# Kernel optimization log

Hardware: AMD Instinct MI355X
Metric: run time of the kernel (lower is better)

Reference implementation:

```python
import jax, jax.numpy as jnp
import numpy as np

N, D_IN, D_BLOCK, D_OUT, E, K = 65536, 128, 256, 128, 8, 2


def setup_inputs() -> dict:
    key = jax.random.key(0)
    ks = jax.random.split(key, 8)
    s_in = 1.0 / np.sqrt(D_IN)
    s_h = 1.0 / np.sqrt(D_BLOCK)
    return {
        "x": jax.random.normal(ks[0], (N, D_IN), jnp.float32),
        "Wg": jax.random.normal(ks[1], (D_IN, E), jnp.float32) * s_in,
        "W1": jax.random.normal(ks[2], (E, D_IN, D_BLOCK), jnp.float32) * s_in,
        "b1": jax.random.normal(ks[3], (E, D_BLOCK), jnp.float32) * 0.01,
        "W2": jax.random.normal(ks[4], (E, D_BLOCK, D_BLOCK), jnp.float32) * s_h,
        "b2": jax.random.normal(ks[5], (E, D_BLOCK), jnp.float32) * 0.01,
        "Wo": jax.random.normal(ks[6], (D_BLOCK, D_OUT), jnp.float32) * s_h,
        "bo": jax.random.normal(ks[7], (D_OUT,), jnp.float32) * 0.01,
    }


def reference(x, Wg, W1, b1, W2, b2, Wo, bo):
    # Router: linear gate -> top-k -> softmax over the k selected logits,
    # scattered back to a dense [N, E] combine-weight matrix (zeros elsewhere).
    logits = x @ Wg                                   # [N, E]
    topv, topi = jax.lax.top_k(logits, K)             # [N, K]
    w_topk = jax.nn.softmax(topv, axis=-1)            # [N, K]
    onehot = jax.nn.one_hot(topi, E, dtype=x.dtype)   # [N, K, E]
    weights = jnp.einsum("nk,nke->ne", w_topk, onehot)  # [N, E]

    # Expert MLPs (n_blocks=2, ReLU, dropout=0 at eval), computed for all
    # experts over all tokens; unselected experts have weight 0, so the
    # weighted combine reproduces the original masked gather/scatter math.
    h = jax.nn.relu(jnp.einsum("nd,edh->enh", x, W1) + b1[:, None, :])   # [E,N,H]
    h = jax.nn.relu(jnp.einsum("enh,ehg->eng", h, W2) + b2[:, None, :])  # [E,N,H]
    y = jnp.einsum("enh,ho->eno", h, Wo) + bo                             # [E,N,O]

    # Weighted scatter-add combine: outs[n] = sum_e weights[n,e] * y[e,n]
    return jnp.einsum("ne,eno->no", weights, y)
```

## Files before the change

### kernel.cpp

```cpp
#include <hip/hip_runtime.h>
#include <math.h>

typedef unsigned short ushort_t;
typedef __attribute__((ext_vector_type(8))) short bf16x8;
typedef __attribute__((ext_vector_type(4))) float f32x4;
typedef __attribute__((ext_vector_type(8))) unsigned short u16x8;

#define N_TOK 65536
#define DIN 128
#define HD 256
#define DOUT 128
#define NEXP 8
#define MT 64
#define MAX_TILES (N_TOK / MT)

__device__ __forceinline__ unsigned short f2bf(float f) {
    union { float f; unsigned int i; } v; v.f = f;
    unsigned int i = v.i;
    return (unsigned short)((i + 0x7FFFu + ((i >> 16) & 1u)) >> 16);
}

__global__ void pack_weights(const float* __restrict__ W1,
                             const float* __restrict__ W2,
                             const float* __restrict__ Wo,
                             ushort_t* __restrict__ wt1f,
                             ushort_t* __restrict__ wt2f,
                             ushort_t* __restrict__ wotf) {
    int id = blockIdx.x * 256 + threadIdx.x;
    const float* src; ushort_t* dst; int Nn, ksteps, c;
    if (id < 32768) {
        int e = id >> 12; c = id & 4095;
        Nn = HD; ksteps = 4; src = W1 + (size_t)e * DIN * HD; dst = wt1f + (size_t)id * 8;
    } else if (id < 98304) {
        int t = id - 32768; int e = t >> 13; c = t & 8191;
        Nn = HD; ksteps = 8; src = W2 + (size_t)e * HD * HD; dst = wt2f + (size_t)t * 8;
    } else {
        int t = id - 98304; c = t;
        Nn = DOUT; ksteps = 8; src = Wo; dst = wotf + (size_t)t * 8;
    }
    int L = c & 63; int kc = c >> 6;
    int kstep = kc % ksteps; int ntile = kc / ksteps;
    int q = L >> 4, m = L & 15;
    int n = ntile * 16 + m; int k0 = kstep * 32 + q * 8;
    u16x8 v;
#pragma unroll
    for (int j = 0; j < 8; j++) v[j] = f2bf(src[(size_t)(k0 + j) * Nn + n]);
    *(u16x8*)dst = v;
}

#define RT_BLOCK 512
#define RT_TPB 64
__global__ __launch_bounds__(RT_BLOCK)
void router_kernel(const float* __restrict__ x,
                   const float* __restrict__ Wg,
                   int* __restrict__ counts,
                   int* __restrict__ list_tok,
                   float* __restrict__ list_w) {
    __shared__ float wgsT[NEXP * 132];
    __shared__ int lcnt[NEXP];
    __shared__ int lbase[NEXP];
    int tid = threadIdx.x;
    if (tid < NEXP) lcnt[tid] = 0;
    for (int i = tid; i < DIN * NEXP; i += RT_BLOCK) {
        int e = i & 7, k = i >> 3;
        wgsT[e * 132 + k] = Wg[i];
    }
    __syncthreads();

    int e = tid & 7;
    int tl = tid >> 3;
    int n = blockIdx.x * RT_TPB + tl;
    const float4* xr = (const float4*)(x + (size_t)n * DIN);
    const float4* wv4 = (const float4*)(wgsT + e * 132);
    float lg = 0.f;
#pragma unroll
    for (int kk = 0; kk < 32; kk++) {
        float4 xv = xr[kk];
        float4 wv = wv4[kk];
        lg += xv.x * wv.x;
        lg += xv.y * wv.y;
        lg += xv.z * wv.z;
        lg += xv.w * wv.w;
    }
    float v0 = lg; int e0 = e;
#pragma unroll
    for (int d = 1; d < 8; d <<= 1) {
        float ov = __shfl_xor(v0, d, 64);
        int oe = __shfl_xor(e0, d, 64);
        if (ov > v0 || (ov == v0 && oe < e0)) { v0 = ov; e0 = oe; }
    }
    float mv = (e == e0) ? -3.0e38f : lg;
    float v1 = mv; int e1 = e;
#pragma unroll
    for (int d = 1; d < 8; d <<= 1) {
        float ov = __shfl_xor(v1, d, 64);
        int oe = __shfl_xor(e1, d, 64);
        if (ov > v1 || (ov == v1 && oe < e1)) { v1 = ov; e1 = oe; }
    }
    float t = expf(v1 - v0);
    float inv = 1.0f / (1.0f + t);
    float w0 = inv, w1 = t * inv;

    bool writer = (e == 0);
    int p0 = 0, p1 = 0;
    if (writer) {
        p0 = atomicAdd(&lcnt[e0], 1);
        p1 = atomicAdd(&lcnt[e1], 1);
    }
    __syncthreads();
    if (tid < NEXP) lbase[tid] = atomicAdd(&counts[tid], lcnt[tid]);
    __syncthreads();
    if (writer) {
        int q0 = lbase[e0] + p0;
        list_tok[e0 * N_TOK + q0] = n;
        list_w[e0 * N_TOK + q0] = w0;
        int q1 = lbase[e1] + p1;
        list_tok[e1 * N_TOK + q1] = n;
        list_w[e1 * N_TOK + q1] = w1;
    }
}

__global__ void init_out(const float* __restrict__ bo, float* __restrict__ out) {
    int gid = blockIdx.x * 256 + threadIdx.x;
    float4 b = ((const float4*)bo)[gid & 31];
    ((float4*)out)[gid] = b;
}

__global__ __launch_bounds__(256, 3)
void expert_kernel(const float* __restrict__ x,
                   const int* __restrict__ counts,
                   const int* __restrict__ list_tok,
                   const float* __restrict__ list_w,
                   const ushort_t* __restrict__ wt1f,
                   const ushort_t* __restrict__ wt2f,
                   const ushort_t* __restrict__ wotf,
                   const float* __restrict__ b1,
                   const float* __restrict__ b2,
                   float* __restrict__ out) {
    int e = blockIdx.x & 7;
    int tile = blockIdx.x >> 3;
    int cnt = counts[e];
    int base = tile * MT;
    if (base >= cnt) return;
    int rows = cnt - base; if (rows > MT) rows = MT;

    __shared__ __align__(16) ushort_t bufA[8192];
    __shared__ __align__(16) ushort_t bufH[16384];
    __shared__ int toks_s[MT];
    __shared__ float wts_s[MT];

    int tid = threadIdx.x;
    int lane = tid & 63;
    int w = tid >> 6;
    int q = lane >> 4;
    int mcol = lane & 15;

    if (tid < MT) {
        int rr = tid < rows ? tid : rows - 1;
        toks_s[tid] = list_tok[(size_t)e * N_TOK + base + rr];
        wts_s[tid] = list_w[(size_t)e * N_TOK + base + rr];
    }
    for (int c = tid; c < 1024; c += 256) {
        int row = c >> 4;
        int kchunk = c & 15;
        int rr = row < rows ? row : rows - 1;
        int tok = list_tok[(size_t)e * N_TOK + base + rr];
        const float4* src = (const float4*)(x + (size_t)tok * DIN + kchunk * 8);
        float4 lo = src[0], hi = src[1];
        u16x8 v;
        v[0] = f2bf(lo.x); v[1] = f2bf(lo.y); v[2] = f2bf(lo.z); v[3] = f2bf(lo.w);
        v[4] = f2bf(hi.x); v[5] = f2bf(hi.y); v[6] = f2bf(hi.z); v[7] = f2bf(hi.w);
        int kstep = kchunk >> 2, qq = kchunk & 3;
        int dchunk = (kstep * 4 + (row >> 4)) * 64 + qq * 16 + (row & 15);
        ((u16x8*)bufA)[dchunk] = v;
    }
    __syncthreads();

    const bf16x8* Albs = (const bf16x8*)bufA;
    const bf16x8* Hlbs = (const bf16x8*)bufH;

    f32x4 acc[4][4];
#pragma unroll
    for (int mt = 0; mt < 4; mt++)
#pragma unroll
        for (int nt = 0; nt < 4; nt++) acc[mt][nt] = (f32x4){0.f, 0.f, 0.f, 0.f};
    const bf16x8* B1 = (const bf16x8*)(wt1f + (size_t)e * 4096 * 8);
#pragma unroll
    for (int kstep = 0; kstep < 4; kstep++) {
        bf16x8 a[4];
#pragma unroll
        for (int mt = 0; mt < 4; mt++) a[mt] = Albs[(kstep * 4 + mt) * 64 + lane];
#pragma unroll
        for (int nt = 0; nt < 4; nt++) {
            bf16x8 b = B1[((w * 4 + nt) * 4 + kstep) * 64 + lane];
#pragma unroll
            for (int mt = 0; mt < 4; mt++)
                acc[mt][nt] = __builtin_amdgcn_mfma_f32_16x16x32_bf16(a[mt], b, acc[mt][nt], 0, 0, 0);
        }
    }
#pragma unroll
    for (int nt = 0; nt < 4; nt++) {
        int nn = (w * 4 + nt) * 16 + mcol;
        float bias = b1[e * HD + nn];
        int kstep = nn >> 5, qq = (nn >> 3) & 3, jj = nn & 7;
#pragma unroll
        for (int mt = 0; mt < 4; mt++) {
#pragma unroll
            for (int r = 0; r < 4; r++) {
                float v = acc[mt][nt][r] + bias;
                v = v > 0.f ? v : 0.f;
                int chunk = (kstep * 4 + mt) * 64 + qq * 16 + q * 4 + r;
                bufH[chunk * 8 + jj] = f2bf(v);
            }
        }
    }
    __syncthreads();

    f32x4 acc2[4][4];
#pragma unroll
    for (int mt = 0; mt < 4; mt++)
#pragma unroll
        for (int nt = 0; nt < 4; nt++) acc2[mt][nt] = (f32x4){0.f, 0.f, 0.f, 0.f};
    const bf16x8* B2 = (const bf16x8*)(wt2f + (size_t)e * 8192 * 8);
#pragma unroll
    for (int kstep = 0; kstep < 8; kstep++) {
        bf16x8 a[4];
#pragma unroll
        for (int mt = 0; mt < 4; mt++) a[mt] = Hlbs[(kstep * 4 + mt) * 64 + lane];
#pragma unroll
        for (int nt = 0; nt < 4; nt++) {
            bf16x8 b = B2[((w * 4 + nt) * 8 + kstep) * 64 + lane];
#pragma unroll
            for (int mt = 0; mt < 4; mt++)
                acc2[mt][nt] = __builtin_amdgcn_mfma_f32_16x16x32_bf16(a[mt], b, acc2[mt][nt], 0, 0, 0);
        }
    }
    __syncthreads();
#pragma unroll
    for (int nt = 0; nt < 4; nt++) {
        int nn = (w * 4 + nt) * 16 + mcol;
        float bias = b2[e * HD + nn];
        int kstep = nn >> 5, qq = (nn >> 3) & 3, jj = nn & 7;
#pragma unroll
        for (int mt = 0; mt < 4; mt++) {
#pragma unroll
            for (int r = 0; r < 4; r++) {
                float v = acc2[mt][nt][r] + bias;
                v = v > 0.f ? v : 0.f;
                int chunk = (kstep * 4 + mt) * 64 + qq * 16 + q * 4 + r;
                bufH[chunk * 8 + jj] = f2bf(v);
            }
        }
    }
    __syncthreads();

    f32x4 acc3[4][2];
#pragma unroll
    for (int mt = 0; mt < 4; mt++)
#pragma unroll
        for (int nt = 0; nt < 2; nt++) acc3[mt][nt] = (f32x4){0.f, 0.f, 0.f, 0.f};
    const bf16x8* B3 = (const bf16x8*)wotf;
#pragma unroll
    for (int kstep = 0; kstep < 8; kstep++) {
        bf16x8 a[4];
#pragma unroll
        for (int mt = 0; mt < 4; mt++) a[mt] = Hlbs[(kstep * 4 + mt) * 64 + lane];
#pragma unroll
        for (int nt = 0; nt < 2; nt++) {
            bf16x8 b = B3[((w * 2 + nt) * 8 + kstep) * 64 + lane];
#pragma unroll
            for (int mt = 0; mt < 4; mt++)
                acc3[mt][nt] = __builtin_amdgcn_mfma_f32_16x16x32_bf16(a[mt], b, acc3[mt][nt], 0, 0, 0);
        }
    }
#pragma unroll
    for (int mt = 0; mt < 4; mt++) {
#pragma unroll
        for (int r = 0; r < 4; r++) {
            int row = mt * 16 + q * 4 + r;
            if (row < rows) {
                int tok = toks_s[row];
                float wgt = wts_s[row];
                float* dst = out + (size_t)tok * DOUT;
#pragma unroll
                for (int nt = 0; nt < 2; nt++) {
                    int col = (w * 2 + nt) * 16 + mcol;
                    atomicAdd(&dst[col], wgt * acc3[mt][nt][r]);
                }
            }
        }
    }
}

extern "C" void kernel_launch(void* const* d_in, const int* in_sizes, int n_in,
                              void* d_out, int out_size, void* d_ws, size_t ws_size,
                              hipStream_t stream) {
    const float* x  = (const float*)d_in[0];
    const float* Wg = (const float*)d_in[1];
    const float* W1 = (const float*)d_in[2];
    const float* b1 = (const float*)d_in[3];
    const float* W2 = (const float*)d_in[4];
    const float* b2 = (const float*)d_in[5];
    const float* Wo = (const float*)d_in[6];
    const float* bo = (const float*)d_in[7];
    float* out = (float*)d_out;

    char* ws = (char*)d_ws;
    size_t off = 0;
    int* counts    = (int*)(ws + off);    off += 256;
    int* list_tok  = (int*)(ws + off);    off += (size_t)NEXP * N_TOK * 4;
    float* list_w  = (float*)(ws + off);  off += (size_t)NEXP * N_TOK * 4;
    ushort_t* wt1f = (ushort_t*)(ws + off); off += (size_t)NEXP * DIN * HD * 2;
    ushort_t* wt2f = (ushort_t*)(ws + off); off += (size_t)NEXP * HD * HD * 2;
    ushort_t* wotf = (ushort_t*)(ws + off); off += (size_t)HD * DOUT * 2;

    hipMemsetAsync(counts, 0, 256, stream);
    pack_weights<<<400, 256, 0, stream>>>(W1, W2, Wo, wt1f, wt2f, wotf);
    router_kernel<<<N_TOK / RT_TPB, RT_BLOCK, 0, stream>>>(x, Wg, counts, list_tok, list_w);
    init_out<<<(N_TOK * DOUT / 4) / 256, 256, 0, stream>>>(bo, out);
    expert_kernel<<<NEXP * MAX_TILES, 256, 0, stream>>>(x, counts, list_tok, list_w,
                                                        wt1f, wt2f, wotf, b1, b2, out);
}
```

Before: 199.6 us.

## Split K across router lanes and use 2x2 warp tiling in expert GEMMs

The router now has each of 8 lanes per token read a distinct 16-float slice of x and compute partial dot products for all 8 experts, then reduce with xor shuffles. Before, all 8 lanes read the full token row. This cuts redundant global reads of x, and the block shrinks to 256 threads with 32 tokens each. The expert kernel switches from warps owning N-slices across all four M-tiles to a 2x2 warp grid: each warp now loads 2 A fragments and 8 B fragments per k-step instead of 4 A and 4 B. That moves per-warp traffic from shared memory to global/L2 weight loads and changes the output atomic pattern.

Measured after the change: 254.5 us. +27.5%, slower.

```diff
diff --git a/kernel.cpp b/kernel.cpp
--- a/kernel.cpp
+++ b/kernel.cpp
@@ -48,9 +48,8 @@
     *(u16x8*)dst = v;
 }
 
-#define RT_BLOCK 512
-#define RT_TPB 64
-__global__ __launch_bounds__(RT_BLOCK)
+#define RT_TPB 32
+__global__ __launch_bounds__(256)
 void router_kernel(const float* __restrict__ x,
                    const float* __restrict__ Wg,
                    int* __restrict__ counts,
@@ -61,47 +60,49 @@
     __shared__ int lbase[NEXP];
     int tid = threadIdx.x;
     if (tid < NEXP) lcnt[tid] = 0;
-    for (int i = tid; i < DIN * NEXP; i += RT_BLOCK) {
+    for (int i = tid; i < DIN * NEXP; i += 256) {
         int e = i & 7, k = i >> 3;
         wgsT[e * 132 + k] = Wg[i];
     }
     __syncthreads();
 
-    int e = tid & 7;
+    int s = tid & 7;
     int tl = tid >> 3;
     int n = blockIdx.x * RT_TPB + tl;
-    const float4* xr = (const float4*)(x + (size_t)n * DIN);
-    const float4* wv4 = (const float4*)(wgsT + e * 132);
-    float lg = 0.f;
-#pragma unroll
-    for (int kk = 0; kk < 32; kk++) {
-        float4 xv = xr[kk];
-        float4 wv = wv4[kk];
-        lg += xv.x * wv.x;
-        lg += xv.y * wv.y;
-        lg += xv.z * wv.z;
-        lg += xv.w * wv.w;
-    }
-    float v0 = lg; int e0 = e;
+
+    const float4* xr = (const float4*)(x + (size_t)n * DIN + s * 16);
+    float4 xv[4];
+#pragma unroll
+    for (int j = 0; j < 4; j++) xv[j] = xr[j];
+
+    float lg[NEXP];
+#pragma unroll
+    for (int e = 0; e < NEXP; e++) {
+        const float4* wp = (const float4*)(wgsT + e * 132 + s * 16);
+        float a = 0.f;
+#pragma unroll
+        for (int j = 0; j < 4; j++) {
+            float4 wv = wp[j];
+            a += xv[j].x * wv.x + xv[j].y * wv.y + xv[j].z * wv.z + xv[j].w * wv.w;
+        }
+        lg[e] = a;
+    }
 #pragma unroll
     for (int d = 1; d < 8; d <<= 1) {
-        float ov = __shfl_xor(v0, d, 64);
-        int oe = __shfl_xor(e0, d, 64);
-        if (ov > v0 || (ov == v0 && oe < e0)) { v0 = ov; e0 = oe; }
-    }
-    float mv = (e == e0) ? -3.0e38f : lg;
-    float v1 = mv; int e1 = e;
-#pragma unroll
-    for (int d = 1; d < 8; d <<= 1) {
-        float ov = __shfl_xor(v1, d, 64);
-        int oe = __shfl_xor(e1, d, 64);
-        if (ov > v1 || (ov == v1 && oe < e1)) { v1 = ov; e1 = oe; }
-    }
+#pragma unroll
+        for (int e = 0; e < NEXP; e++) lg[e] += __shfl_xor(lg[e], d, 64);
+    }
+    int e0 = 0; float v0 = lg[0];
+#pragma unroll
+    for (int e = 1; e < NEXP; e++) if (lg[e] > v0) { v0 = lg[e]; e0 = e; }
+    int e1 = -1; float v1 = -3.0e38f;
+#pragma unroll
+    for (int e = 0; e < NEXP; e++) if (e != e0 && lg[e] > v1) { v1 = lg[e]; e1 = e; }
     float t = expf(v1 - v0);
     float inv = 1.0f / (1.0f + t);
     float w0 = inv, w1 = t * inv;
 
-    bool writer = (e == 0);
+    bool writer = (s == 0);
     int p0 = 0, p1 = 0;
     if (writer) {
         p0 = atomicAdd(&lcnt[e0], 1);
@@ -152,6 +153,8 @@
     int tid = threadIdx.x;
     int lane = tid & 63;
     int w = tid >> 6;
+    int mw = w >> 1;
+    int nw = w & 1;
     int q = lane >> 4;
     int mcol = lane & 15;
 
@@ -179,35 +182,37 @@
     const bf16x8* Albs = (const bf16x8*)bufA;
     const bf16x8* Hlbs = (const bf16x8*)bufH;
 
-    f32x4 acc[4][4];
-#pragma unroll
-    for (int mt = 0; mt < 4; mt++)
-#pragma unroll
-        for (int nt = 0; nt < 4; nt++) acc[mt][nt] = (f32x4){0.f, 0.f, 0.f, 0.f};
+    f32x4 acc[2][8];
+#pragma unroll
+    for (int mtl = 0; mtl < 2; mtl++)
+#pragma unroll
+        for (int nt = 0; nt < 8; nt++) acc[mtl][nt] = (f32x4){0.f, 0.f, 0.f, 0.f};
     const bf16x8* B1 = (const bf16x8*)(wt1f + (size_t)e * 4096 * 8);
 #pragma unroll
     for (int kstep = 0; kstep < 4; kstep++) {
-        bf16x8 a[4];
-#pragma unroll
-        for (int mt = 0; mt < 4; mt++) a[mt] = Albs[(kstep * 4 + mt) * 64 + lane];
-#pragma unroll
-        for (int nt = 0; nt < 4; nt++) {
-            bf16x8 b = B1[((w * 4 + nt) * 4 + kstep) * 64 + lane];
-#pragma unroll
-            for (int mt = 0; mt < 4; mt++)
-                acc[mt][nt] = __builtin_amdgcn_mfma_f32_16x16x32_bf16(a[mt], b, acc[mt][nt], 0, 0, 0);
-        }
-    }
-#pragma unroll
-    for (int nt = 0; nt < 4; nt++) {
-        int nn = (w * 4 + nt) * 16 + mcol;
+        bf16x8 a[2];
+#pragma unroll
+        for (int mtl = 0; mtl < 2; mtl++)
+            a[mtl] = Albs[(kstep * 4 + mw * 2 + mtl) * 64 + lane];
+#pragma unroll
+        for (int nt = 0; nt < 8; nt++) {
+            bf16x8 b = B1[((nw * 8 + nt) * 4 + kstep) * 64 + lane];
+#pragma unroll
+            for (int mtl = 0; mtl < 2; mtl++)
+                acc[mtl][nt] = __builtin_amdgcn_mfma_f32_16x16x32_bf16(a[mtl], b, acc[mtl][nt], 0, 0, 0);
+        }
+    }
+#pragma unroll
+    for (int nt = 0; nt < 8; nt++) {
+        int nn = nw * 128 + nt * 16 + mcol;
         float bias = b1[e * HD + nn];
         int kstep = nn >> 5, qq = (nn >> 3) & 3, jj = nn & 7;
 #pragma unroll
-        for (int mt = 0; mt < 4; mt++) {
+        for (int mtl = 0; mtl < 2; mtl++) {
+            int mt = mw * 2 + mtl;
 #pragma unroll
             for (int r = 0; r < 4; r++) {
-                float v = acc[mt][nt][r] + bias;
+                float v = acc[mtl][nt][r] + bias;
                 v = v > 0.f ? v : 0.f;
                 int chunk = (kstep * 4 + mt) * 64 + qq * 16 + q * 4 + r;
                 bufH[chunk * 8 + jj] = f2bf(v);
@@ -216,36 +221,38 @@
     }
     __syncthreads();
 
-    f32x4 acc2[4][4];
-#pragma unroll
-    for (int mt = 0; mt < 4; mt++)
-#pragma unroll
-        for (int nt = 0; nt < 4; nt++) acc2[mt][nt] = (f32x4){0.f, 0.f, 0.f, 0.f};
+    f32x4 acc2[2][8];
+#pragma unroll
+    for (int mtl = 0; mtl < 2; mtl++)
+#pragma unroll
+        for (int nt = 0; nt < 8; nt++) acc2[mtl][nt] = (f32x4){0.f, 0.f, 0.f, 0.f};
     const bf16x8* B2 = (const bf16x8*)(wt2f + (size_t)e * 8192 * 8);
 #pragma unroll
     for (int kstep = 0; kstep < 8; kstep++) {
-        bf16x8 a[4];
-#pragma unroll
-        for (int mt = 0; mt < 4; mt++) a[mt] = Hlbs[(kstep * 4 + mt) * 64 + lane];
-#pragma unroll
-        for (int nt = 0; nt < 4; nt++) {
-            bf16x8 b = B2[((w * 4 + nt) * 8 + kstep) * 64 + lane];
-#pragma unroll
-            for (int mt = 0; mt < 4; mt++)
-                acc2[mt][nt] = __builtin_amdgcn_mfma_f32_16x16x32_bf16(a[mt], b, acc2[mt][nt], 0, 0, 0);
-        }
-    }
-    __syncthreads();
-#pragma unroll
-    for (int nt = 0; nt < 4; nt++) {
-        int nn = (w * 4 + nt) * 16 + mcol;
+        bf16x8 a[2];
+#pragma unroll
+        for (int mtl = 0; mtl < 2; mtl++)
+            a[mtl] = Hlbs[(kstep * 4 + mw * 2 + mtl) * 64 + lane];
+#pragma unroll
+        for (int nt = 0; nt < 8; nt++) {
+            bf16x8 b = B2[((nw * 8 + nt) * 8 + kstep) * 64 + lane];
+#pragma unroll
+            for (int mtl = 0; mtl < 2; mtl++)
+                acc2[mtl][nt] = __builtin_amdgcn_mfma_f32_16x16x32_bf16(a[mtl], b, acc2[mtl][nt], 0, 0, 0);
+        }
+    }
+    __syncthreads();
+#pragma unroll
+    for (int nt = 0; nt < 8; nt++) {
+        int nn = nw * 128 + nt * 16 + mcol;
         float bias = b2[e * HD + nn];
         int kstep = nn >> 5, qq = (nn >> 3) & 3, jj = nn & 7;
 #pragma unroll
-        for (int mt = 0; mt < 4; mt++) {
+        for (int mtl = 0; mtl < 2; mtl++) {
+            int mt = mw * 2 + mtl;
 #pragma unroll
             for (int r = 0; r < 4; r++) {
-                float v = acc2[mt][nt][r] + bias;
+                float v = acc2[mtl][nt][r] + bias;
                 v = v > 0.f ? v : 0.f;
                 int chunk = (kstep * 4 + mt) * 64 + qq * 16 + q * 4 + r;
                 bufH[chunk * 8 + jj] = f2bf(v);
@@ -254,27 +261,29 @@
     }
     __syncthreads();
 
-    f32x4 acc3[4][2];
-#pragma unroll
-    for (int mt = 0; mt < 4; mt++)
-#pragma unroll
-        for (int nt = 0; nt < 2; nt++) acc3[mt][nt] = (f32x4){0.f, 0.f, 0.f, 0.f};
+    f32x4 acc3[2][4];
+#pragma unroll
+    for (int mtl = 0; mtl < 2; mtl++)
+#pragma unroll
+        for (int nt = 0; nt < 4; nt++) acc3[mtl][nt] = (f32x4){0.f, 0.f, 0.f, 0.f};
     const bf16x8* B3 = (const bf16x8*)wotf;
 #pragma unroll
     for (int kstep = 0; kstep < 8; kstep++) {
-        bf16x8 a[4];
-#pragma unroll
-        for (int mt = 0; mt < 4; mt++) a[mt] = Hlbs[(kstep * 4 + mt) * 64 + lane];
-#pragma unroll
-        for (int nt = 0; nt < 2; nt++) {
-            bf16x8 b = B3[((w * 2 + nt) * 8 + kstep) * 64 + lane];
-#pragma unroll
-            for (int mt = 0; mt < 4; mt++)
-                acc3[mt][nt] = __builtin_amdgcn_mfma_f32_16x16x32_bf16(a[mt], b, acc3[mt][nt], 0, 0, 0);
-        }
-    }
-#pragma unroll
-    for (int mt = 0; mt < 4; mt++) {
+        bf16x8 a[2];
+#pragma unroll
+        for (int mtl = 0; mtl < 2; mtl++)
+            a[mtl] = Hlbs[(kstep * 4 + mw * 2 + mtl) * 64 + lane];
+#pragma unroll
+        for (int nt = 0; nt < 4; nt++) {
+            bf16x8 b = B3[((nw * 4 + nt) * 8 + kstep) * 64 + lane];
+#pragma unroll
+            for (int mtl = 0; mtl < 2; mtl++)
+                acc3[mtl][nt] = __builtin_amdgcn_mfma_f32_16x16x32_bf16(a[mtl], b, acc3[mtl][nt], 0, 0, 0);
+        }
+    }
+#pragma unroll
+    for (int mtl = 0; mtl < 2; mtl++) {
+        int mt = mw * 2 + mtl;
 #pragma unroll
         for (int r = 0; r < 4; r++) {
             int row = mt * 16 + q * 4 + r;
@@ -283,9 +292,9 @@
                 float wgt = wts_s[row];
                 float* dst = out + (size_t)tok * DOUT;
 #pragma unroll
-                for (int nt = 0; nt < 2; nt++) {
-                    int col = (w * 2 + nt) * 16 + mcol;
-                    atomicAdd(&dst[col], wgt * acc3[mt][nt][r]);
+                for (int nt = 0; nt < 4; nt++) {
+                    int col = (nw * 4 + nt) * 16 + mcol;
+                    atomicAdd(&dst[col], wgt * acc3[mtl][nt][r]);
                 }
             }
         }
@@ -316,7 +325,7 @@
 
     hipMemsetAsync(counts, 0, 256, stream);
     pack_weights<<<400, 256, 0, stream>>>(W1, W2, Wo, wt1f, wt2f, wotf);
-    router_kernel<<<N_TOK / RT_TPB, RT_BLOCK, 0, stream>>>(x, Wg, counts, list_tok, list_w);
+    router_kernel<<<N_TOK / RT_TPB, 256, 0, stream>>>(x, Wg, counts, list_tok, list_w);
     init_out<<<(N_TOK * DOUT / 4) / 256, 256, 0, stream>>>(bo, out);
     expert_kernel<<<NEXP * MAX_TILES, 256, 0, stream>>>(x, counts, list_tok, list_w,
                                                         wt1f, wt2f, wotf, b1, b2, out);
```

## Segment router token lists per expert to cut global atomic contention

Applied to the files above, without the earlier changes.

Token lists are split into 32 segments per expert, each with its own counter, so router blocks append through 256 counters instead of 8 global ones. The expert kernel grid now covers expert × segment × tile, and the memset is folded into pack_weights. The router is also restructured: each thread computes a partial dot product over 16 features for all 8 experts, reduced with shuffles, then picks top-2 with a sequential scan. This adds more partially filled 64-row tiles and therefore more wasted MMA work. It also assumes no segment ever receives more than 2048 tokens.

Result: slower. 213.8 us (+7.1%).

```diff
diff --git a/kernel.cpp b/kernel.cpp
--- a/kernel.cpp
+++ b/kernel.cpp
@@ -12,7 +12,9 @@
 #define DOUT 128
 #define NEXP 8
 #define MT 64
-#define MAX_TILES (N_TOK / MT)
+#define NSEG 32
+#define SEGCAP 2048
+#define SEGTILES (SEGCAP / MT)
 
 __device__ __forceinline__ unsigned short f2bf(float f) {
     union { float f; unsigned int i; } v; v.f = f;
@@ -25,7 +27,9 @@
                              const float* __restrict__ Wo,
                              ushort_t* __restrict__ wt1f,
                              ushort_t* __restrict__ wt2f,
-                             ushort_t* __restrict__ wotf) {
+                             ushort_t* __restrict__ wotf,
+                             int* __restrict__ segcnt) {
+    if (blockIdx.x == 0) segcnt[threadIdx.x] = 0;
     int id = blockIdx.x * 256 + threadIdx.x;
     const float* src; ushort_t* dst; int Nn, ksteps, c;
     if (id < 32768) {
@@ -48,12 +52,11 @@
     *(u16x8*)dst = v;
 }
 
-#define RT_BLOCK 512
-#define RT_TPB 64
-__global__ __launch_bounds__(RT_BLOCK)
+#define RT_TPB 32
+__global__ __launch_bounds__(256)
 void router_kernel(const float* __restrict__ x,
                    const float* __restrict__ Wg,
-                   int* __restrict__ counts,
+                   int* __restrict__ segcnt,
                    int* __restrict__ list_tok,
                    float* __restrict__ list_w) {
     __shared__ float wgsT[NEXP * 132];
@@ -61,62 +64,67 @@
     __shared__ int lbase[NEXP];
     int tid = threadIdx.x;
     if (tid < NEXP) lcnt[tid] = 0;
-    for (int i = tid; i < DIN * NEXP; i += RT_BLOCK) {
+    for (int i = tid; i < DIN * NEXP; i += 256) {
         int e = i & 7, k = i >> 3;
         wgsT[e * 132 + k] = Wg[i];
     }
     __syncthreads();
 
-    int e = tid & 7;
+    int s = tid & 7;
     int tl = tid >> 3;
     int n = blockIdx.x * RT_TPB + tl;
-    const float4* xr = (const float4*)(x + (size_t)n * DIN);
-    const float4* wv4 = (const float4*)(wgsT + e * 132);
-    float lg = 0.f;
-#pragma unroll
-    for (int kk = 0; kk < 32; kk++) {
-        float4 xv = xr[kk];
-        float4 wv = wv4[kk];
-        lg += xv.x * wv.x;
-        lg += xv.y * wv.y;
-        lg += xv.z * wv.z;
-        lg += xv.w * wv.w;
-    }
-    float v0 = lg; int e0 = e;
+
+    const float4* xr = (const float4*)(x + (size_t)n * DIN + s * 16);
+    float4 xv[4];
+#pragma unroll
+    for (int j = 0; j < 4; j++) xv[j] = xr[j];
+
+    float lg[NEXP];
+#pragma unroll
+    for (int e = 0; e < NEXP; e++) {
+        const float4* wp = (const float4*)(wgsT + e * 132 + s * 16);
+        float a = 0.f;
+#pragma unroll
+        for (int j = 0; j < 4; j++) {
+            float4 wv = wp[j];
+            a += xv[j].x * wv.x + xv[j].y * wv.y + xv[j].z * wv.z + xv[j].w * wv.w;
+        }
+        lg[e] = a;
+    }
 #pragma unroll
     for (int d = 1; d < 8; d <<= 1) {
-        float ov = __shfl_xor(v0, d, 64);
-        int oe = __shfl_xor(e0, d, 64);
-        if (ov > v0 || (ov == v0 && oe < e0)) { v0 = ov; e0 = oe; }
-    }
-    float mv = (e == e0) ? -3.0e38f : lg;
-    float v1 = mv; int e1 = e;
-#pragma unroll
-    for (int d = 1; d < 8; d <<= 1) {
-        float ov = __shfl_xor(v1, d, 64);
-        int oe = __shfl_xor(e1, d, 64);
-        if (ov > v1 || (ov == v1 && oe < e1)) { v1 = ov; e1 = oe; }
-    }
+#pragma unroll
+        for (int e = 0; e < NEXP; e++) lg[e] += __shfl_xor(lg[e], d, 64);
+    }
+    int e0 = 0; float v0 = lg[0];
+#pragma unroll
+    for (int e = 1; e < NEXP; e++) if (lg[e] > v0) { v0 = lg[e]; e0 = e; }
+    int e1 = -1; float v1 = -3.0e38f;
+#pragma unroll
+    for (int e = 0; e < NEXP; e++) if (e != e0 && lg[e] > v1) { v1 = lg[e]; e1 = e; }
     float t = expf(v1 - v0);
     float inv = 1.0f / (1.0f + t);
     float w0 = inv, w1 = t * inv;
 
-    bool writer = (e == 0);
+    bool writer = (s == 0);
     int p0 = 0, p1 = 0;
     if (writer) {
         p0 = atomicAdd(&lcnt[e0], 1);
         p1 = atomicAdd(&lcnt[e1], 1);
     }
     __syncthreads();
-    if (tid < NEXP) lbase[tid] = atomicAdd(&counts[tid], lcnt[tid]);
+    int c = blockIdx.x & (NSEG - 1);
+    if (tid < NEXP) lbase[tid] = atomicAdd(&segcnt[tid * NSEG + c], lcnt[tid]);
     __syncthreads();
     if (writer) {
         int q0 = lbase[e0] + p0;
-        list_tok[e0 * N_TOK + q0] = n;
-        list_w[e0 * N_TOK + q0] = w0;
+        int idx0 = (e0 * NSEG + c) * SEGCAP + q0;
+        list_tok[idx0] = n;
+        list_w[idx0] = w0;
         int q1 = lbase[e1] + p1;
-        list_tok[e1 * N_TOK + q1] = n;
-        list_w[e1 * N_TOK + q1] = w1;
+        int idx1 = (e1 * NSEG + c) * SEGCAP + q1;
+        list_tok[idx1] = n;
+        list_w[idx1] = w1;
     }
 }
 
@@ -128,7 +136,7 @@
 
 __global__ __launch_bounds__(256, 3)
 void expert_kernel(const float* __restrict__ x,
-                   const int* __restrict__ counts,
+                   const int* __restrict__ segcnt,
                    const int* __restrict__ list_tok,
                    const float* __restrict__ list_w,
                    const ushort_t* __restrict__ wt1f,
@@ -137,12 +145,15 @@
                    const float* __restrict__ b1,
                    const float* __restrict__ b2,
                    float* __restrict__ out) {
-    int e = blockIdx.x & 7;
-    int tile = blockIdx.x >> 3;
-    int cnt = counts[e];
-    int base = tile * MT;
+    int bid = blockIdx.x;
+    int e = bid & 7;
+    int c = (bid >> 3) & (NSEG - 1);
+    int t = bid >> 8;
+    int cnt = segcnt[e * NSEG + c];
+    int base = t * MT;
     if (base >= cnt) return;
     int rows = cnt - base; if (rows > MT) rows = MT;
+    int lidx = (e * NSEG + c) * SEGCAP + base;
 
     __shared__ __align__(16) ushort_t bufA[8192];
     __shared__ __align__(16) ushort_t bufH[16384];
@@ -157,14 +168,14 @@
 
     if (tid < MT) {
         int rr = tid < rows ? tid : rows - 1;
-        toks_s[tid] = list_tok[(size_t)e * N_TOK + base + rr];
-        wts_s[tid] = list_w[(size_t)e * N_TOK + base + rr];
-    }
-    for (int c = tid; c < 1024; c += 256) {
-        int row = c >> 4;
-        int kchunk = c & 15;
+        toks_s[tid] = list_tok[lidx + rr];
+        wts_s[tid] = list_w[lidx + rr];
+    }
+    for (int cc = tid; cc < 1024; cc += 256) {
+        int row = cc >> 4;
+        int kchunk = cc & 15;
         int rr = row < rows ? row : rows - 1;
-        int tok = list_tok[(size_t)e * N_TOK + base + rr];
+        int tok = list_tok[lidx + rr];
         const float4* src = (const float4*)(x + (size_t)tok * DIN + kchunk * 8);
         float4 lo = src[0], hi = src[1];
         u16x8 v;
@@ -307,17 +318,16 @@
 
     char* ws = (char*)d_ws;
     size_t off = 0;
-    int* counts    = (int*)(ws + off);    off += 256;
-    int* list_tok  = (int*)(ws + off);    off += (size_t)NEXP * N_TOK * 4;
-    float* list_w  = (float*)(ws + off);  off += (size_t)NEXP * N_TOK * 4;
+    int* segcnt    = (int*)(ws + off);    off += 1024;
+    int* list_tok  = (int*)(ws + off);    off += (size_t)NEXP * NSEG * SEGCAP * 4;
+    float* list_w  = (float*)(ws + off);  off += (size_t)NEXP * NSEG * SEGCAP * 4;
     ushort_t* wt1f = (ushort_t*)(ws + off); off += (size_t)NEXP * DIN * HD * 2;
     ushort_t* wt2f = (ushort_t*)(ws + off); off += (size_t)NEXP * HD * HD * 2;
     ushort_t* wotf = (ushort_t*)(ws + off); off += (size_t)HD * DOUT * 2;
 
-    hipMemsetAsync(counts, 0, 256, stream);
-    pack_weights<<<400, 256, 0, stream>>>(W1, W2, Wo, wt1f, wt2f, wotf);
-    router_kernel<<<N_TOK / RT_TPB, RT_BLOCK, 0, stream>>>(x, Wg, counts, list_tok, list_w);
+    pack_weights<<<400, 256, 0, stream>>>(W1, W2, Wo, wt1f, wt2f, wotf, segcnt);
+    router_kernel<<<N_TOK / RT_TPB, 256, 0, stream>>>(x, Wg, segcnt, list_tok, list_w);
     init_out<<<(N_TOK * DOUT / 4) / 256, 256, 0, stream>>>(bo, out);
-    expert_kernel<<<NEXP * MAX_TILES, 256, 0, stream>>>(x, counts, list_tok, list_w,
-                                                        wt1f, wt2f, wotf, b1, b2, out);
-}
+    expert_kernel<<<NEXP * NSEG * SEGTILES, 256, 0, stream>>>(x, segcnt, list_tok, list_w,
+                                                              wt1f, wt2f, wotf, b1, b2, out);
+}
```
